# Performance work log

Measured on AMD Instinct MI355X. Metric: run time of the kernel, lower is better.

The kernel has to match this reference:

```python
import jax, jax.numpy as jnp
import numpy as np

N = 1024          # number of nodes
E = 32768         # number of edges
S = 4             # num_scales
STEPS = 31        # num_steps
MIN_SIGMA = 0.1
MAX_SIGMA = 3.0
EPS = 1e-12       # F.normalize eps


def setup_inputs() -> dict:
    key = jax.random.key(0)
    k1, k2 = jax.random.split(key, 2)
    coords = jax.random.normal(k1, (N, 3), dtype=jnp.float32)
    edge_index = jax.random.randint(k2, (2, E), 0, N, dtype=jnp.int64)
    # learned parameter, initialized exactly as in the module
    log_sigmas = jnp.linspace(jnp.log(jnp.float32(MIN_SIGMA)),
                              jnp.log(jnp.float32(MAX_SIGMA)), S).astype(jnp.float32)
    return {"coords": coords, "log_sigmas": log_sigmas, "edge_index": edge_index}


def reference(coords, log_sigmas, edge_index):
    n = coords.shape[0]
    # pairwise squared euclidean distances (cdist(..)^2)  [N,N]
    diff = coords[:, None, :] - coords[None, :, :]
    d2 = jnp.sum(diff * diff, axis=-1)

    sigmas = jnp.sort(jnp.exp(log_sigmas))                       # [S]
    w = jnp.exp(-d2[None, :, :] / (2.0 * sigmas[:, None, None] ** 2))  # [S,N,N]
    eye = jnp.eye(n, dtype=w.dtype)
    w = w * (1.0 - eye)                                          # zero diagonal
    row_sum = jnp.sum(w, axis=2, keepdims=True)                  # L1 row norm (w>=0)
    P = w / jnp.maximum(row_sum, EPS)                            # row-stochastic, 0 rows -> 0

    ei, ej = edge_index[0], edge_index[1]

    def step(P_k, _):
        P_k = P_k @ P                                            # batched [S,N,N] GEMM
        diag = jnp.diagonal(P_k, axis1=1, axis2=2)               # [S,N]
        edge = P_k[:, ei, ej]                                    # [S,E]
        return P_k, (diag, edge)

    P0 = jnp.broadcast_to(eye, P.shape)
    _, (diags, edges) = jax.lax.scan(step, P0, None, length=STEPS)
    # diags: [STEPS,S,N] -> node features [N, S*STEPS] (scale-major, step-minor)
    node_features = jnp.transpose(diags, (2, 1, 0)).reshape(n, S * STEPS)
    edge_features = jnp.transpose(edges, (2, 1, 0)).reshape(ei.shape[0], S * STEPS)
    return node_features, edge_features
```

## Files before the change

### kernel.cpp

```cpp
#include <hip/hip_runtime.h>

#define N 1024
#define NE 32768
#define S 4
#define STEPS 31
#define FEAT (S * STEPS)
#define PLANE ((size_t)S * N * N)
#define MAXT 192

typedef short short8 __attribute__((ext_vector_type(8)));
typedef short short4v __attribute__((ext_vector_type(4)));
typedef float f32x4 __attribute__((ext_vector_type(4)));

__device__ __forceinline__ ushort f2bf(float x) {
    union { float f; unsigned u; } v; v.f = x;
    unsigned r = v.u + 0x7fffu + ((v.u >> 16) & 1u);
    return (ushort)(r >> 16);
}
__device__ __forceinline__ float bf2f(ushort h) {
    union { unsigned u; float f; } v; v.u = ((unsigned)h) << 16;
    return v.f;
}

__device__ __forceinline__ void gload16(const ushort* g, ushort* l) {
    __builtin_amdgcn_global_load_lds(
        (const __attribute__((address_space(1))) unsigned int*)g,
        (__attribute__((address_space(3))) unsigned int*)l, 16, 0, 0);
}

__global__ __launch_bounds__(256) void build_P(const float* __restrict__ coords,
                                               const float* __restrict__ log_sigmas,
                                               ushort* __restrict__ Oh,
                                               ushort* __restrict__ Ol)
{
    const int i   = blockIdx.x;
    const int tid = threadIdx.x;

    float sg[S];
#pragma unroll
    for (int s = 0; s < S; ++s) sg[s] = expf(log_sigmas[s]);
#define CSWP(a, b) { float lo = fminf(sg[a], sg[b]); float hi = fmaxf(sg[a], sg[b]); sg[a] = lo; sg[b] = hi; }
    CSWP(0, 1) CSWP(2, 3) CSWP(0, 2) CSWP(1, 3) CSWP(1, 2)
#undef CSWP
    float inv2s2[S];
#pragma unroll
    for (int s = 0; s < S; ++s) inv2s2[s] = 1.0f / (2.0f * sg[s] * sg[s]);

    const float cx = coords[3 * i + 0];
    const float cy = coords[3 * i + 1];
    const float cz = coords[3 * i + 2];

    float w[4][S];
    float part[S] = {0.f, 0.f, 0.f, 0.f};
#pragma unroll
    for (int c = 0; c < 4; ++c) {
        const int j = tid + c * 256;
        const float dx = cx - coords[3 * j + 0];
        const float dy = cy - coords[3 * j + 1];
        const float dz = cz - coords[3 * j + 2];
        const float d2 = dx * dx + dy * dy + dz * dz;
#pragma unroll
        for (int s = 0; s < S; ++s) {
            const float v = (j == i) ? 0.0f : expf(-d2 * inv2s2[s]);
            w[c][s] = v;
            part[s] += v;
        }
    }

    __shared__ float red[S][256];
#pragma unroll
    for (int s = 0; s < S; ++s) red[s][tid] = part[s];
    __syncthreads();
    for (int st = 128; st > 0; st >>= 1) {
        if (tid < st) {
#pragma unroll
            for (int s = 0; s < S; ++s) red[s][tid] += red[s][tid + st];
        }
        __syncthreads();
    }

    float invden[S];
#pragma unroll
    for (int s = 0; s < S; ++s) invden[s] = 1.0f / fmaxf(red[s][0], 1e-12f);

#pragma unroll
    for (int c = 0; c < 4; ++c) {
        const int j = tid + c * 256;
#pragma unroll
        for (int s = 0; s < S; ++s) {
            const float p = w[c][s] * invden[s];
            const size_t off = ((size_t)s * N + i) * N + j;
            const ushort h = f2bf(p);
            Oh[off] = h;
            Ol[off] = f2bf(p - bf2f(h));
        }
    }
}

__global__ __launch_bounds__(256) void transpose_hl(const ushort* __restrict__ Xh,
                                                    const ushort* __restrict__ Xl,
                                                    ushort* __restrict__ Yh,
                                                    ushort* __restrict__ Yl)
{
    __shared__ float tile[64][65];
    const size_t zb = (size_t)blockIdx.z * N * N;
    const int tr = blockIdx.y * 64, tc = blockIdx.x * 64;
    const int tid = threadIdx.x;
    const int c  = tid & 63;
    const int r0 = tid >> 6;
#pragma unroll
    for (int i = 0; i < 16; ++i) {
        const int r = r0 + i * 4;
        const size_t idx = zb + (size_t)(tr + r) * N + tc + c;
        tile[r][c] = bf2f(Xh[idx]) + bf2f(Xl[idx]);
    }
    __syncthreads();
#pragma unroll
    for (int i = 0; i < 16; ++i) {
        const int r = r0 + i * 4;
        const size_t idx = zb + (size_t)(tc + r) * N + tr + c;
        const float x = tile[c][r];
        const ushort h = f2bf(x);
        Yh[idx] = h;
        if (Yl) Yl[idx] = f2bf(x - bf2f(h));
    }
}

template <bool SPLIT>
__device__ __forceinline__ void gemm_body(const ushort* __restrict__ Ah,
                                          const ushort* __restrict__ Al,
                                          const ushort* __restrict__ BTh,
                                          const ushort* __restrict__ BTl,
                                          ushort* __restrict__ Ch,
                                          ushort* __restrict__ Cl,
                                          ushort* __restrict__ CTh,
                                          ushort* __restrict__ CTl,
                                          int id)
{
    constexpr int NP = SPLIT ? 4 : 2;
    __shared__ ushort smem[4][NP][128 * 32];
    const int tid  = threadIdx.x;
    const int w    = tid >> 6;
    const int lane = tid & 63;
    const int wr   = w >> 1;
    const int wc   = w & 1;

    const int yrow = id & 7;
    const int rest = id >> 3;
    const int xcol = rest & 7;
    const int z    = rest >> 3;
    const size_t zb = (size_t)z * N * N;
    const int tr = yrow * 128;
    const int tc = xcol * 128;

    const ushort* gA0 = Ah  + zb + (size_t)tr * N;
    const ushort* gA1 = SPLIT ? (Al  + zb + (size_t)tr * N) : nullptr;
    const ushort* gB0 = BTh + zb + (size_t)tc * N;
    const ushort* gB1 = SPLIT ? (BTl + zb + (size_t)tc * N) : nullptr;

    f32x4 acc[2][4] = {};

    auto STAGE = [&](int bufi, int k0) __attribute__((always_inline)) {
        const int row = tid >> 2;
        const int kg  = (tid & 3) ^ ((row >> 1) & 3);
        const size_t go = (size_t)row * N + k0 + kg * 8;
        const int lb = w * 512;
        gload16(gA0 + go, &smem[bufi][0][lb]);
        if constexpr (SPLIT) {
            gload16(gA1 + go, &smem[bufi][1][lb]);
            gload16(gB0 + go, &smem[bufi][2][lb]);
            gload16(gB1 + go, &smem[bufi][3][lb]);
        } else {
            gload16(gB0 + go, &smem[bufi][1][lb]);
        }
    };

    const int lrow = lane & 15;
    const int lkg  = lane >> 4;

    auto COMPUTE = [&](int bufi) __attribute__((always_inline)) {
        short8 ah[2], al[2], bh[4], bl[4];
#pragma unroll
        for (int m = 0; m < 2; ++m) {
            const int arow = wr * 32 + m * 16 + lrow;
            const int aoff = arow * 32 + ((lkg ^ ((arow >> 1) & 3)) << 3);
            ah[m] = *(const short8*)&smem[bufi][0][aoff];
            if constexpr (SPLIT) al[m] = *(const short8*)&smem[bufi][1][aoff];
        }
#pragma unroll
        for (int n = 0; n < 4; ++n) {
            const int brow = wc * 64 + n * 16 + lrow;
            const int boff = brow * 32 + ((lkg ^ ((brow >> 1) & 3)) << 3);
            if constexpr (SPLIT) {
                bh[n] = *(const short8*)&smem[bufi][2][boff];
                bl[n] = *(const short8*)&smem[bufi][3][boff];
            } else {
                bh[n] = *(const short8*)&smem[bufi][1][boff];
            }
        }
        __builtin_amdgcn_s_setprio(1);
#pragma unroll
        for (int m = 0; m < 2; ++m)
#pragma unroll
            for (int n = 0; n < 4; ++n) {
                acc[m][n] = __builtin_amdgcn_mfma_f32_16x16x32_bf16(ah[m], bh[n], acc[m][n], 0, 0, 0);
                if constexpr (SPLIT) {
                    acc[m][n] = __builtin_amdgcn_mfma_f32_16x16x32_bf16(ah[m], bl[n], acc[m][n], 0, 0, 0);
                    acc[m][n] = __builtin_amdgcn_mfma_f32_16x16x32_bf16(al[m], bh[n], acc[m][n], 0, 0, 0);
                }
            }
        __builtin_amdgcn_s_setprio(0);
    };

    STAGE(0, 0);
    STAGE(1, 32);
#pragma unroll 1
    for (int t = 0; t < 32; ++t) {
        __builtin_amdgcn_sched_barrier(0);
        if (t < 30) {
            STAGE((t + 2) & 3, (t + 2) * 32);
            if constexpr (SPLIT) asm volatile("s_waitcnt vmcnt(8)" ::: "memory");
            else                 asm volatile("s_waitcnt vmcnt(4)" ::: "memory");
        } else if (t == 30) {
            if constexpr (SPLIT) asm volatile("s_waitcnt vmcnt(4)" ::: "memory");
            else                 asm volatile("s_waitcnt vmcnt(2)" ::: "memory");
        } else {
            asm volatile("s_waitcnt vmcnt(0)" ::: "memory");
        }
        __builtin_amdgcn_s_barrier();
        __builtin_amdgcn_sched_barrier(0);
        COMPUTE(t & 3);
        __builtin_amdgcn_sched_barrier(0);
    }

#pragma unroll
    for (int m = 0; m < 2; ++m)
#pragma unroll
    for (int n = 0; n < 4; ++n) {
        const f32x4 v = acc[m][n];
        ushort hs[4], ls[4];
#pragma unroll
        for (int r = 0; r < 4; ++r) {
            const float x = v[r];
            hs[r] = f2bf(x);
            ls[r] = f2bf(x - bf2f(hs[r]));
        }
        const int row0 = tr + wr * 32 + m * 16 + lkg * 4;
        const int col  = tc + wc * 64 + n * 16 + lrow;
        if (Ch) {
#pragma unroll
            for (int r = 0; r < 4; ++r) {
                const size_t idx = zb + (size_t)(row0 + r) * N + col;
                Ch[idx] = hs[r];
                if (Cl) Cl[idx] = ls[r];
            }
        }
        if (CTh) {
            short4v hv;
            hv[0] = (short)hs[0]; hv[1] = (short)hs[1];
            hv[2] = (short)hs[2]; hv[3] = (short)hs[3];
            *(short4v*)&CTh[zb + (size_t)col * N + row0] = hv;
            if (CTl) {
                short4v lv;
                lv[0] = (short)ls[0]; lv[1] = (short)ls[1];
                lv[2] = (short)ls[2]; lv[3] = (short)ls[3];
                *(short4v*)&CTl[zb + (size_t)col * N + row0] = lv;
            }
        }
    }
}

template <bool SPLIT>
__global__ __launch_bounds__(512) void gemm_tile(const ushort* __restrict__ Ah,
                                                 const ushort* __restrict__ Al,
                                                 const ushort* __restrict__ BTh,
                                                 const ushort* __restrict__ BTl,
                                                 ushort* __restrict__ Ch,
                                                 ushort* __restrict__ Cl,
                                                 ushort* __restrict__ CTh,
                                                 ushort* __restrict__ CTl)
{
    gemm_body<SPLIT>(Ah, Al, BTh, BTl, Ch, Cl, CTh, CTl, blockIdx.x);
}

__global__ __launch_bounds__(512) void gemm_leaf(
    const ushort* A0, const ushort* B0, ushort* C0, ushort* T0,
    const ushort* A1, const ushort* B1, ushort* C1, ushort* T1,
    const ushort* A2, const ushort* B2, ushort* C2, ushort* T2,
    const ushort* A3, const ushort* B3, ushort* C3, ushort* T3)
{
    const int op = blockIdx.x >> 8;
    const int id = blockIdx.x & 255;
    const ushort* A; const ushort* B; ushort* C; ushort* T;
    if      (op == 0) { A = A0; B = B0; C = C0; T = T0; }
    else if (op == 1) { A = A1; B = B1; C = C1; T = T1; }
    else if (op == 2) { A = A2; B = B2; C = C2; T = T2; }
    else              { A = A3; B = B3; C = C3; T = T3; }
    gemm_body<false>(A, nullptr, B, nullptr, C, nullptr, T, nullptr, id);
}

__global__ __launch_bounds__(256) void gather_hl(const ushort* __restrict__ Ph,
                                                 const ushort* __restrict__ Pl,
                                                 const int* __restrict__ eidx,
                                                 float* __restrict__ out,
                                                 int t)
{
    const int tid = blockIdx.x * blockDim.x + threadIdx.x;
    const int ND = S * N;
    if (tid < ND) {
        const int s = tid >> 10;
        const int n = tid & (N - 1);
        const size_t off = ((size_t)s * N + n) * N + n;
        float v = bf2f(Ph[off]);
        if (Pl) v += bf2f(Pl[off]);
        out[(size_t)n * FEAT + s * STEPS + t] = v;
    } else {
        const int idx = tid - ND;
        if (idx >= S * NE) return;
        const int s = idx >> 15;
        const int e = idx & (NE - 1);
        const int i = eidx[e];
        const int j = eidx[NE + e];
        const size_t off = ((size_t)s * N + i) * N + j;
        float v = bf2f(Ph[off]);
        if (Pl) v += bf2f(Pl[off]);
        out[(size_t)N * FEAT + (size_t)e * FEAT + s * STEPS + t] = v;
    }
}

__global__ __launch_bounds__(256) void zero_aux(int* __restrict__ p, int n)
{
    for (int i = blockIdx.x * 256 + threadIdx.x; i < n; i += gridDim.x * 256) p[i] = 0;
}

__global__ __launch_bounds__(256) void edge_hist(const int* __restrict__ eidx,
                                                 int* __restrict__ hist)
{
    const int e = blockIdx.x * 256 + threadIdx.x;
    if (e < NE) atomicAdd(&hist[eidx[NE + e]], 1);
}

__global__ __launch_bounds__(1024) void scan1024(const int* __restrict__ hist,
                                                 int* __restrict__ offs)
{
    __shared__ int tmp[1024];
    const int t = threadIdx.x;
    tmp[t] = hist[t];
    __syncthreads();
    for (int d = 1; d < 1024; d <<= 1) {
        int v = (t >= d) ? tmp[t - d] : 0;
        __syncthreads();
        tmp[t] += v;
        __syncthreads();
    }
    offs[t + 1] = tmp[t];
    if (t == 0) offs[0] = 0;
}

__global__ __launch_bounds__(256) void edge_scatter(const int* __restrict__ eidx,
                                                    const int* __restrict__ offs,
                                                    int* __restrict__ cursor,
                                                    int* __restrict__ perm)
{
    const int e = blockIdx.x * 256 + threadIdx.x;
    if (e < NE) {
        const int j = eidx[NE + e];
        const int pos = atomicAdd(&cursor[j], 1);
        perm[offs[j] + pos] = e;
    }
}

__global__ __launch_bounds__(256) void extract_k(const ushort* __restrict__ BT,
                                                 const ushort* __restrict__ A12,
                                                 const ushort* __restrict__ A24,
                                                 const int* __restrict__ eidx,
                                                 const int* __restrict__ perm,
                                                 const int* __restrict__ offs,
                                                 float* __restrict__ out)
{
    const int id = blockIdx.x;
    const int s  = (id & 7) >> 1;
    const int j  = (id >> 3) * 2 + (id & 1);
    const int tid  = threadIdx.x;
    const int wave = tid >> 6;
    const int lane = tid & 63;

    __shared__ __align__(16) ushort bt[12][1032];
    __shared__ int tlist[MAXT];
    __shared__ int elist[MAXT];

    const int base  = offs[j];
    const int cnt   = min(offs[j + 1] - base, MAXT - 1);
    const int ntask = cnt + 1;
    const int ngrp  = (ntask + 15) >> 4;

    for (int t0 = tid; t0 < MAXT; t0 += 256) {
        int e = -2, i = j;
        if (t0 < cnt)       { e = perm[base + t0]; i = eidx[e]; }
        else if (t0 == cnt) { e = -1; }
        tlist[t0] = i;
        elist[t0] = e;
    }

    const size_t rowbase = ((size_t)s * N + j) * N;
    for (int c = tid; c < 12 * 128; c += 256) {
        const int b  = c >> 7;
        const int ch = c & 127;
        const short8 v = *(const short8*)&BT[(size_t)b * PLANE + rowbase + ch * 8];
        *(short8*)&bt[b][ch * 8] = v;
    }
    __syncthreads();

    for (int t0 = tid; t0 < ntask; t0 += 256) {
        const int i = tlist[t0];
        const int e = elist[t0];
        const size_t obase = (e >= 0)
            ? ((size_t)N * FEAT + (size_t)e * FEAT + (size_t)s * STEPS)
            : ((size_t)j * FEAT + (size_t)s * STEPS);
#pragma unroll
        for (int b = 0; b < 12; ++b)
            out[obase + b] = bf2f(bt[b][i]);
    }

    const int nidx = lane & 15;
    const int koff = (lane >> 4) * 8;
    const ushort* bt_ptr = &bt[nidx < 12 ? nidx : 0][koff];

    for (int g = wave; g < ngrp; g += 4) {
        const int i = tlist[g * 16 + nidx];
        const size_t abase = ((size_t)s * N + i) * N + koff;
        const ushort* pa0 = A12 + abase;
        const ushort* pa1 = A24 + abase;

        f32x4 acc0 = {}, acc1 = {};
#pragma unroll 4
        for (int ks = 0; ks < 32; ++ks) {
            const short8 bf  = *(const short8*)(bt_ptr + ks * 32);
            const short8 af0 = *(const short8*)(pa0 + ks * 32);
            const short8 af1 = *(const short8*)(pa1 + ks * 32);
            acc0 = __builtin_amdgcn_mfma_f32_16x16x32_bf16(af0, bf, acc0, 0, 0, 0);
            acc1 = __builtin_amdgcn_mfma_f32_16x16x32_bf16(af1, bf, acc1, 0, 0, 0);
        }

        if (nidx < 12) {
            const int m0 = (lane >> 4) * 4;
#pragma unroll
            for (int r = 0; r < 4; ++r) {
                const int e = elist[g * 16 + m0 + r];
                if (e >= -1) {
                    const size_t obase = (e >= 0)
                        ? ((size_t)N * FEAT + (size_t)e * FEAT + (size_t)s * STEPS)
                        : ((size_t)j * FEAT + (size_t)s * STEPS);
                    out[obase + 12 + nidx] = acc0[r];
                    if (nidx < 7)
                        out[obase + 24 + nidx] = acc1[r];
                }
            }
        }
    }
}

extern "C" void kernel_launch(void* const* d_in, const int* in_sizes, int n_in,
                              void* d_out, int out_size, void* d_ws, size_t ws_size,
                              hipStream_t stream)
{
    const float* coords     = (const float*)d_in[0];
    const float* log_sigmas = (const float*)d_in[1];
    const int*   eidx       = (const int*)d_in[2];
    float*       out        = (float*)d_out;

    ushort* W = (ushort*)d_ws;
    const dim3 tgrid(16, 16, S);
    ushort* const NUL = nullptr;
#define PS(k) (W + (size_t)(k) * PLANE)

    const size_t AUX_INTS = 1024 + 1024 + 1025 + NE;
    const size_t NEED_A   = 15 * PLANE * sizeof(ushort) + AUX_INTS * sizeof(int);

    if (ws_size >= NEED_A) {
        int* hist   = (int*)(W + 15 * PLANE);
        int* cursor = hist + 1024;
        int* offs   = cursor + 1024;
        int* perm   = offs + 1025;

        zero_aux<<<8, 256, 0, stream>>>(hist, 2048);
        edge_hist<<<NE / 256, 256, 0, stream>>>(eidx, hist);
        scan1024<<<1, 1024, 0, stream>>>(hist, offs);
        edge_scatter<<<NE / 256, 256, 0, stream>>>(eidx, offs, cursor, perm);

        build_P<<<N, 256, 0, stream>>>(coords, log_sigmas, PS(12), PS(13));
        transpose_hl<<<tgrid, 256, 0, stream>>>(PS(12), PS(13), PS(0), PS(4));

        gemm_tile<true><<<256, 512, 0, stream>>>(PS(12), PS(13), PS(0), PS(4),
                                                 PS(6), PS(10), PS(1), PS(5));
        gemm_tile<true><<<256, 512, 0, stream>>>(PS(6), PS(10), PS(1), PS(5),
                                                 PS(11), PS(8), PS(3), PS(9));
        gemm_leaf<<<768, 512, 0, stream>>>(
            PS(6), PS(0), NUL, PS(2),
            PS(11), PS(0), NUL, PS(4),
            PS(11), PS(1), NUL, PS(5),
            NUL, NUL, NUL, NUL);
        gemm_tile<true><<<256, 512, 0, stream>>>(PS(11), PS(8), PS(3), PS(9),
                                                 PS(12), NUL, PS(7), NUL);
        gemm_leaf<<<1024, 512, 0, stream>>>(
            PS(11), PS(2), NUL, PS(6),
            PS(12), PS(0), NUL, PS(8),
            PS(12), PS(1), NUL, PS(9),
            PS(12), PS(2), NUL, PS(10));
        gemm_tile<false><<<256, 512, 0, stream>>>(PS(12), NUL, PS(3), NUL,
                                                  PS(13), NUL, PS(11), NUL);
        gemm_tile<false><<<256, 512, 0, stream>>>(PS(13), NUL, PS(11), NUL,
                                                  PS(14), NUL, NUL, NUL);

        extract_k<<<N * S, 256, 0, stream>>>(W, PS(13), PS(14), eidx, perm, offs, out);
    } else {
        ushort* ping_h = PS(0); ushort* ping_l = PS(1);
        ushort* pong_h = PS(2); ushort* pong_l = PS(3);
        ushort* bt_h   = PS(4); ushort* bt_l   = PS(5);
        const int gather_blocks = (S * N + S * NE + 255) / 256;

        build_P<<<N, 256, 0, stream>>>(coords, log_sigmas, ping_h, ping_l);
        gather_hl<<<gather_blocks, 256, 0, stream>>>(ping_h, ping_l, eidx, out, 0);
        transpose_hl<<<tgrid, 256, 0, stream>>>(ping_h, ping_l, bt_h, bt_l);

        ushort* cur_h = ping_h; ushort* cur_l = ping_l;
        ushort* nxt_h = pong_h; ushort* nxt_l = pong_l;
        for (int k = 2; k <= STEPS; ++k) {
            gemm_tile<true><<<256, 512, 0, stream>>>(cur_h, cur_l, bt_h, bt_l,
                                                     nxt_h, nxt_l, NUL, NUL);
            gather_hl<<<gather_blocks, 256, 0, stream>>>(nxt_h, nxt_l, eidx, out, k - 1);
            ushort* th = cur_h; ushort* tl = cur_l;
            cur_h = nxt_h; cur_l = nxt_l; nxt_h = th; nxt_l = tl;
        }
    }
#undef PS
}
```

Measured before the change: 347.1 us.

## Quantize extraction operands to int8 and merge step-12 GEMM into leaf batch

Restructures the power-of-P schedule so the P^12 product is computed inside a five-op leaf launch rather than a separate dependent GEMM, removing one serial GEMM launch. The final extraction kernel now reads int8-quantized P^12/P^24 rows (per-row max scaling) and uses int8 MFMA with fp32 rescaling, halving the bytes gathered per row and using the higher-throughput int8 path. It adds a quantization pass and reduces the numerical precision of the high-power features, which may or may not stay within tolerance.

```diff
diff --git a/kernel.cpp b/kernel.cpp
--- a/kernel.cpp
+++ b/kernel.cpp
@@ -11,6 +11,7 @@
 typedef short short8 __attribute__((ext_vector_type(8)));
 typedef short short4v __attribute__((ext_vector_type(4)));
 typedef float f32x4 __attribute__((ext_vector_type(4)));
+typedef int int4v __attribute__((ext_vector_type(4)));
 
 __device__ __forceinline__ ushort f2bf(float x) {
     union { float f; unsigned u; } v; v.f = x;
@@ -287,7 +288,8 @@
     const ushort* A0, const ushort* B0, ushort* C0, ushort* T0,
     const ushort* A1, const ushort* B1, ushort* C1, ushort* T1,
     const ushort* A2, const ushort* B2, ushort* C2, ushort* T2,
-    const ushort* A3, const ushort* B3, ushort* C3, ushort* T3)
+    const ushort* A3, const ushort* B3, ushort* C3, ushort* T3,
+    const ushort* A4, const ushort* B4, ushort* C4, ushort* T4)
 {
     const int op = blockIdx.x >> 8;
     const int id = blockIdx.x & 255;
@@ -295,8 +297,45 @@
     if      (op == 0) { A = A0; B = B0; C = C0; T = T0; }
     else if (op == 1) { A = A1; B = B1; C = C1; T = T1; }
     else if (op == 2) { A = A2; B = B2; C = C2; T = T2; }
-    else              { A = A3; B = B3; C = C3; T = T3; }
+    else if (op == 3) { A = A3; B = B3; C = C3; T = T3; }
+    else              { A = A4; B = B4; C = C4; T = T4; }
     gemm_body<false>(A, nullptr, B, nullptr, C, nullptr, T, nullptr, id);
+}
+
+__global__ __launch_bounds__(128) void quant8(const ushort* __restrict__ X12,
+                                              const ushort* __restrict__ X24,
+                                              unsigned char* __restrict__ Q,
+                                              float* __restrict__ sc)
+{
+    const int id  = blockIdx.x;
+    const int pl  = id >> 12;
+    const int row = id & 4095;
+    const int tid = threadIdx.x;
+    const ushort* src = (pl ? X24 : X12) + (size_t)row * N;
+    unsigned char* dst = Q + (size_t)pl * PLANE + (size_t)row * N;
+
+    float v[8];
+    const short8 x = ((const short8*)src)[tid];
+    float mx = 0.0f;
+#pragma unroll
+    for (int e = 0; e < 8; ++e) { v[e] = bf2f((ushort)x[e]); mx = fmaxf(mx, v[e]); }
+#pragma unroll
+    for (int d = 1; d < 64; d <<= 1) mx = fmaxf(mx, __shfl_xor(mx, d, 64));
+    __shared__ float wmx[2];
+    if ((tid & 63) == 0) wmx[tid >> 6] = mx;
+    __syncthreads();
+    mx = fmaxf(fmaxf(wmx[0], wmx[1]), 1e-30f);
+
+    const float inv = 127.0f / mx;
+    uint2 q;
+    q.x = 0; q.y = 0;
+#pragma unroll
+    for (int e = 0; e < 4; ++e) {
+        q.x |= ((unsigned)(int)(v[e] * inv + 0.5f)) << (e * 8);
+        q.y |= ((unsigned)(int)(v[4 + e] * inv + 0.5f)) << (e * 8);
+    }
+    ((uint2*)dst)[tid] = q;
+    if (tid == 0) sc[id] = mx * (1.0f / 127.0f);
 }
 
 __global__ __launch_bounds__(256) void gather_hl(const ushort* __restrict__ Ph,
@@ -370,9 +409,13 @@
     }
 }
 
-__global__ __launch_bounds__(256) void extract_k(const ushort* __restrict__ BT,
-                                                 const ushort* __restrict__ A12,
-                                                 const ushort* __restrict__ A24,
+__global__ __launch_bounds__(256) void extract_k(const ushort* __restrict__ BT18,
+                                                 const ushort* __restrict__ bt9p,
+                                                 const ushort* __restrict__ bt10p,
+                                                 const ushort* __restrict__ bt11p,
+                                                 const ushort* __restrict__ bt12p,
+                                                 const unsigned char* __restrict__ Q,
+                                                 const float* __restrict__ sc,
                                                  const int* __restrict__ eidx,
                                                  const int* __restrict__ perm,
                                                  const int* __restrict__ offs,
@@ -386,8 +429,15 @@
     const int lane = tid & 63;
 
     __shared__ __align__(16) ushort bt[12][1032];
+    __shared__ __align__(16) unsigned char btq[12][1040];
     __shared__ int tlist[MAXT];
     __shared__ int elist[MAXT];
+    __shared__ float saA[MAXT], saC[MAXT];
+    __shared__ int   rowmaxi[12];
+    __shared__ float sbq[12], sbinv[12];
+
+    if (tid < 12) rowmaxi[tid] = 0;
+    __syncthreads();
 
     const int base  = offs[j];
     const int cnt   = min(offs[j + 1] - base, MAXT - 1);
@@ -406,11 +456,41 @@
     for (int c = tid; c < 12 * 128; c += 256) {
         const int b  = c >> 7;
         const int ch = c & 127;
-        const short8 v = *(const short8*)&BT[(size_t)b * PLANE + rowbase + ch * 8];
+        const ushort* q = (b < 8) ? (BT18 + (size_t)b * PLANE)
+                        : (b == 8 ? bt9p : b == 9 ? bt10p : b == 10 ? bt11p : bt12p);
+        const short8 v = *(const short8*)&q[rowbase + ch * 8];
         *(short8*)&bt[b][ch * 8] = v;
-    }
-    __syncthreads();
-
+        float mx = 0.0f;
+#pragma unroll
+        for (int x = 0; x < 8; ++x) mx = fmaxf(mx, bf2f((ushort)v[x]));
+        atomicMax(&rowmaxi[b], __float_as_int(mx));
+    }
+    __syncthreads();
+
+    if (tid < 12) {
+        const float rm = fmaxf(__int_as_float(rowmaxi[tid]), 1e-30f);
+        sbq[tid]   = rm * (1.0f / 127.0f);
+        sbinv[tid] = 127.0f / rm;
+    }
+    __syncthreads();
+
+    for (int c = tid; c < 12 * 128; c += 256) {
+        const int b  = c >> 7;
+        const int ch = c & 127;
+        const float inv = sbinv[b];
+        uint2 q; q.x = 0; q.y = 0;
+#pragma unroll
+        for (int x = 0; x < 4; ++x) {
+            q.x |= ((unsigned)(int)(bf2f(bt[b][ch * 8 + x]) * inv + 0.5f)) << (x * 8);
+            q.y |= ((unsigned)(int)(bf2f(bt[b][ch * 8 + 4 + x]) * inv + 0.5f)) << (x * 8);
+        }
+        *(uint2*)&btq[b][ch * 8] = q;
+    }
+    for (int t0 = tid; t0 < MAXT; t0 += 256) {
+        const int i = tlist[t0];
+        saA[t0] = sc[s * N + i];
+        saC[t0] = sc[S * N + s * N + i];
+    }
     for (int t0 = tid; t0 < ntask; t0 += 256) {
         const int i = tlist[t0];
         const int e = elist[t0];
@@ -421,39 +501,42 @@
         for (int b = 0; b < 12; ++b)
             out[obase + b] = bf2f(bt[b][i]);
     }
+    __syncthreads();
 
     const int nidx = lane & 15;
-    const int koff = (lane >> 4) * 8;
-    const ushort* bt_ptr = &bt[nidx < 12 ? nidx : 0][koff];
+    const int koff = (lane >> 4) * 16;
+    const unsigned char* btq_ptr = &btq[nidx < 12 ? nidx : 0][koff];
 
     for (int g = wave; g < ngrp; g += 4) {
         const int i = tlist[g * 16 + nidx];
         const size_t abase = ((size_t)s * N + i) * N + koff;
-        const ushort* pa0 = A12 + abase;
-        const ushort* pa1 = A24 + abase;
-
-        f32x4 acc0 = {}, acc1 = {};
-#pragma unroll 4
-        for (int ks = 0; ks < 32; ++ks) {
-            const short8 bf  = *(const short8*)(bt_ptr + ks * 32);
-            const short8 af0 = *(const short8*)(pa0 + ks * 32);
-            const short8 af1 = *(const short8*)(pa1 + ks * 32);
-            acc0 = __builtin_amdgcn_mfma_f32_16x16x32_bf16(af0, bf, acc0, 0, 0, 0);
-            acc1 = __builtin_amdgcn_mfma_f32_16x16x32_bf16(af1, bf, acc1, 0, 0, 0);
+        const unsigned char* pa0 = Q + abase;
+        const unsigned char* pa1 = Q + PLANE + abase;
+
+        int4v acc0 = {}, acc1 = {};
+#pragma unroll 8
+        for (int ks = 0; ks < 16; ++ks) {
+            const int4v bv  = *(const int4v*)(btq_ptr + ks * 64);
+            const int4v av0 = *(const int4v*)(pa0 + ks * 64);
+            const int4v av1 = *(const int4v*)(pa1 + ks * 64);
+            acc0 = __builtin_amdgcn_mfma_i32_16x16x64_i8(av0, bv, acc0, 0, 0, 0);
+            acc1 = __builtin_amdgcn_mfma_i32_16x16x64_i8(av1, bv, acc1, 0, 0, 0);
         }
 
         if (nidx < 12) {
             const int m0 = (lane >> 4) * 4;
+            const float sb = sbq[nidx];
 #pragma unroll
             for (int r = 0; r < 4; ++r) {
-                const int e = elist[g * 16 + m0 + r];
+                const int task = g * 16 + m0 + r;
+                const int e = elist[task];
                 if (e >= -1) {
                     const size_t obase = (e >= 0)
                         ? ((size_t)N * FEAT + (size_t)e * FEAT + (size_t)s * STEPS)
                         : ((size_t)j * FEAT + (size_t)s * STEPS);
-                    out[obase + 12 + nidx] = acc0[r];
+                    out[obase + 12 + nidx] = (float)acc0[r] * saA[task] * sb;
                     if (nidx < 7)
-                        out[obase + 24 + nidx] = acc1[r];
+                        out[obase + 24 + nidx] = (float)acc1[r] * saC[task] * sb;
                 }
             }
         }
@@ -474,7 +557,7 @@
     ushort* const NUL = nullptr;
 #define PS(k) (W + (size_t)(k) * PLANE)
 
-    const size_t AUX_INTS = 1024 + 1024 + 1025 + NE;
+    const size_t AUX_INTS = 1024 + 1024 + 1025 + NE + 2 * S * N;
     const size_t NEED_A   = 15 * PLANE * sizeof(ushort) + AUX_INTS * sizeof(int);
 
     if (ws_size >= NEED_A) {
@@ -482,6 +565,7 @@
         int* cursor = hist + 1024;
         int* offs   = cursor + 1024;
         int* perm   = offs + 1025;
+        float* sc   = (float*)(perm + NE);
 
         zero_aux<<<8, 256, 0, stream>>>(hist, 2048);
         edge_hist<<<NE / 256, 256, 0, stream>>>(eidx, hist);
@@ -489,30 +573,34 @@
         edge_scatter<<<NE / 256, 256, 0, stream>>>(eidx, offs, cursor, perm);
 
         build_P<<<N, 256, 0, stream>>>(coords, log_sigmas, PS(12), PS(13));
-        transpose_hl<<<tgrid, 256, 0, stream>>>(PS(12), PS(13), PS(0), PS(4));
-
-        gemm_tile<true><<<256, 512, 0, stream>>>(PS(12), PS(13), PS(0), PS(4),
-                                                 PS(6), PS(10), PS(1), PS(5));
-        gemm_tile<true><<<256, 512, 0, stream>>>(PS(6), PS(10), PS(1), PS(5),
-                                                 PS(11), PS(8), PS(3), PS(9));
+        transpose_hl<<<tgrid, 256, 0, stream>>>(PS(12), PS(13), PS(0), PS(8));
+
+        gemm_tile<true><<<256, 512, 0, stream>>>(PS(12), PS(13), PS(0), PS(8),
+                                                 PS(9), PS(10), PS(1), PS(11));
+        gemm_tile<true><<<256, 512, 0, stream>>>(PS(9), PS(10), PS(1), PS(11),
+                                                 PS(12), PS(13), PS(3), PS(14));
         gemm_leaf<<<768, 512, 0, stream>>>(
-            PS(6), PS(0), NUL, PS(2),
-            PS(11), PS(0), NUL, PS(4),
-            PS(11), PS(1), NUL, PS(5),
+            PS(9), PS(0), NUL, PS(2),
+            PS(12), PS(0), NUL, PS(4),
+            PS(12), PS(1), NUL, PS(5),
+            NUL, NUL, NUL, NUL,
             NUL, NUL, NUL, NUL);
-        gemm_tile<true><<<256, 512, 0, stream>>>(PS(11), PS(8), PS(3), PS(9),
-                                                 PS(12), NUL, PS(7), NUL);
-        gemm_leaf<<<1024, 512, 0, stream>>>(
-            PS(11), PS(2), NUL, PS(6),
-            PS(12), PS(0), NUL, PS(8),
-            PS(12), PS(1), NUL, PS(9),
-            PS(12), PS(2), NUL, PS(10));
-        gemm_tile<false><<<256, 512, 0, stream>>>(PS(12), NUL, PS(3), NUL,
-                                                  PS(13), NUL, PS(11), NUL);
-        gemm_tile<false><<<256, 512, 0, stream>>>(PS(13), NUL, PS(11), NUL,
-                                                  PS(14), NUL, NUL, NUL);
-
-        extract_k<<<N * S, 256, 0, stream>>>(W, PS(13), PS(14), eidx, perm, offs, out);
+        gemm_tile<true><<<256, 512, 0, stream>>>(PS(12), PS(13), PS(3), PS(14),
+                                                 PS(9), NUL, PS(7), NUL);
+        gemm_leaf<<<1280, 512, 0, stream>>>(
+            PS(12), PS(2), NUL, PS(6),
+            PS(9), PS(0), NUL, PS(10),
+            PS(9), PS(1), NUL, PS(11),
+            PS(9), PS(2), NUL, PS(13),
+            PS(9), PS(3), PS(14), PS(8));
+        gemm_tile<false><<<256, 512, 0, stream>>>(PS(14), NUL, PS(8), NUL,
+                                                  PS(12), NUL, NUL, NUL);
+        quant8<<<2 * S * N, 128, 0, stream>>>(PS(14), PS(12),
+                                              (unsigned char*)PS(9), sc);
+
+        extract_k<<<N * S, 256, 0, stream>>>(W, PS(10), PS(11), PS(13), PS(8),
+                                             (const unsigned char*)PS(9), sc,
+                                             eidx, perm, offs, out);
     } else {
         ushort* ping_h = PS(0); ushort* ping_l = PS(1);
         ushort* pong_h = PS(2); ushort* pong_l = PS(3);
```

Result: faster. 328.3 us (-5.4%).
